# Kernel tuning notes

Hardware: AMD Instinct MI355X
Metric: run time of the kernel (lower is better)

## Reference

```python
import jax, jax.numpy as jnp
import numpy as np

N_HEAD = 16


def setup_inputs() -> dict:
    key = jax.random.key(0)
    ks = jax.random.split(key, 5)
    B, T, C = 4, 4096, 2048
    H = N_HEAD
    x = jax.random.normal(ks[0], (B, T, C), dtype=jnp.float32)
    # torch Linear weights are (out_features, in_features); bias=False
    Wa = jax.random.normal(ks[1], (C, C), dtype=jnp.float32) * 0.02
    Wp = jax.random.normal(ks[2], (C, C), dtype=jnp.float32) * 0.02
    temp = jnp.ones((H, 1), dtype=jnp.float32)
    denom_bias = jnp.zeros((H, T, 1), dtype=jnp.float32)  # block_size == T
    return {"x": x, "Wa": Wa, "Wp": Wp, "temp": temp, "denom_bias": denom_bias}


def reference(x, Wa, Wp, temp, denom_bias):
    B, T, C = x.shape
    H = N_HEAD
    D = C // H
    # c_attn (no bias): y = x @ Wa^T
    w = jnp.einsum('btc,oc->bto', x, Wa)
    w = w.reshape(B, T, H, D).transpose(0, 2, 1, 3)  # (B,H,T,D)
    w_sq = w * w
    # running second-moment denominator along time
    denom = jnp.maximum(jnp.cumsum(w_sq, axis=2), 1e-12)
    w_normed = w_sq / denom + denom_bias[:, :T, :]          # (B,H,T,D)
    tmp = jnp.sum(w_normed, axis=-1) * temp                 # (B,H,T), temp (H,1) broadcasts
    Pi = jax.nn.softmax(tmp, axis=1)                        # softmax over heads
    # token-statistics attention: running Pi-weighted mean of w_sq
    dots = jnp.cumsum(w_sq * Pi[..., None], axis=2) / (jnp.cumsum(Pi, axis=-1) + 1e-8)[..., None]
    attn = 1.0 / (1.0 + dots)                               # (B,H,T,D)
    y = -(w * Pi[..., None]) * attn                         # (B,H,T,D)
    y = y.transpose(0, 2, 1, 3).reshape(B, T, C)
    # c_proj (no bias)
    y = jnp.einsum('btc,oc->bto', y, Wp)
    return y
```

## Files before the change

### kernel.cpp

```cpp
#include <hip/hip_runtime.h>
#include <hip/hip_bf16.h>
#include <stdint.h>

#define BB 4
#define TT 4096
#define CC 2048
#define HH 16
#define DD 128
#define MM (BB*TT)
#define KK CC
#define NNx CC
#define NTP 16

#define NCH 128
#define CHL (TT/NCH)

typedef unsigned short u16;
typedef unsigned int   u32;
typedef __bf16 bf16x8 __attribute__((ext_vector_type(8)));
typedef float  f32x4  __attribute__((ext_vector_type(4)));

__device__ __forceinline__ float bf2f(u32 lo) {
  union { u32 u; float f; } z; z.u = lo << 16; return z.f;
}
__device__ __forceinline__ u16 f2bf(float f) {
  union { float f; u32 u; } z; z.f = f;
  u32 u = z.u;
  return (u16)((u + 0x7FFFu + ((u >> 16) & 1u)) >> 16);
}
__device__ __forceinline__ void unpack8(uint4 v, float* a) {
  a[0]=bf2f(v.x&0xffffu); a[1]=bf2f(v.x>>16);
  a[2]=bf2f(v.y&0xffffu); a[3]=bf2f(v.y>>16);
  a[4]=bf2f(v.z&0xffffu); a[5]=bf2f(v.z>>16);
  a[6]=bf2f(v.w&0xffffu); a[7]=bf2f(v.w>>16);
}

__global__ void cvt_f32_bf16(const float* __restrict__ in, u16* __restrict__ out, long n) {
  long i = ((long)blockIdx.x * blockDim.x + threadIdx.x) * 8;
  if (i >= n) return;
  float4 v0 = *(const float4*)(in + i);
  float4 v1 = *(const float4*)(in + i + 4);
  uint4 o;
  o.x = (u32)f2bf(v0.x) | ((u32)f2bf(v0.y) << 16);
  o.y = (u32)f2bf(v0.z) | ((u32)f2bf(v0.w) << 16);
  o.z = (u32)f2bf(v1.x) | ((u32)f2bf(v1.y) << 16);
  o.w = (u32)f2bf(v1.z) | ((u32)f2bf(v1.w) << 16);
  *(uint4*)(out + i) = o;
}

__device__ __forceinline__ void gload16(const void* g, void* l) {
  __builtin_amdgcn_global_load_lds(
      (__attribute__((address_space(1))) void*)g,
      (__attribute__((address_space(3))) void*)l, 16, 0, 0);
}

template<int OUTF32, int EPI>
__global__ __launch_bounds__(512, 2)
void gemm256(const u16* __restrict__ A, const u16* __restrict__ Bm,
             float* __restrict__ Cf, u16* __restrict__ Cb,
             float* __restrict__ S1)
{
  __shared__ u16 As[4][8192];
  __shared__ u16 Bs[4][8192];
  const int tid  = threadIdx.x;
  const int wid  = tid >> 6;
  const int lane = tid & 63;
  const int wm = wid >> 2, wn = wid & 3;
  const int fr = lane & 15, kg = lane >> 4;
  const int orig = blockIdx.x;
  const int nid  = ((orig & 7) << 6) | (orig >> 3);
  const int m0 = (nid >> 3) * 256;
  const int n0 = (nid & 7) * 256;

  const int srow = tid >> 2;
  const int sc   = (tid & 3) ^ ((srow >> 1) & 3);
  const u16* gA0 = A  + (size_t)(m0 + srow) * KK + sc * 8;
  const u16* gA1 = gA0 + (size_t)128 * KK;
  const u16* gB0 = Bm + (size_t)(n0 + srow) * KK + sc * 8;
  const u16* gB1 = gB0 + (size_t)128 * KK;
  const int ldst0 = wid * 512;
  const int ldst1 = 4096 + wid * 512;

  const int cs    = kg ^ ((fr >> 1) & 3);
  const int abase = (wm * 128 + fr) * 32 + cs * 8;
  const int bbase = (wn * 64  + fr) * 32 + cs * 8;

  f32x4 acc[8][4];
  #pragma unroll
  for (int i = 0; i < 8; ++i)
    #pragma unroll
    for (int j = 0; j < 4; ++j) acc[i][j] = (f32x4){0.f,0.f,0.f,0.f};

  auto stA = [&](int slot, int ko) {
    gload16(gA0 + ko, &As[slot][ldst0]);
    gload16(gA1 + ko, &As[slot][ldst1]);
  };
  auto stB = [&](int slot, int ko) {
    gload16(gB0 + ko, &Bs[slot][ldst0]);
    gload16(gB1 + ko, &Bs[slot][ldst1]);
  };

  stA(0, 0);  stB(0, 0);
  stA(1, 32); stB(1, 32);
  stA(2, 64); stB(2, 64);
  asm volatile("s_waitcnt vmcnt(8)" ::: "memory");
  __builtin_amdgcn_s_barrier();

  bf16x8 av[4], bv[4];

#define PH(CSLOT, MH, LOADB, STMT, DOWAIT) do {                               \
    _Pragma("unroll")                                                         \
    for (int f = 0; f < 4; ++f)                                               \
      av[f] = *(const bf16x8*)&As[CSLOT][abase + ((MH)*64 + f*16)*32];        \
    if (LOADB) {                                                              \
      _Pragma("unroll")                                                       \
      for (int f = 0; f < 4; ++f)                                             \
        bv[f] = *(const bf16x8*)&Bs[CSLOT][bbase + f*16*32];                  \
    }                                                                         \
    STMT;                                                                     \
    if (DOWAIT) asm volatile("s_waitcnt vmcnt(8)" ::: "memory");              \
    __builtin_amdgcn_s_barrier();                                             \
    __builtin_amdgcn_s_setprio(1);                                            \
    _Pragma("unroll")                                                         \
    for (int f = 0; f < 4; ++f)                                               \
      _Pragma("unroll")                                                       \
      for (int n = 0; n < 4; ++n)                                             \
        acc[(MH)*4+f][n] = __builtin_amdgcn_mfma_f32_16x16x32_bf16(          \
            av[f], bv[n], acc[(MH)*4+f][n], 0, 0, 0);                         \
    __builtin_amdgcn_s_setprio(0);                                            \
    __builtin_amdgcn_s_barrier();                                             \
  } while (0)

  for (int it = 0; it < NTP; ++it) {
    const int kb = it * 128;
    const bool nx = (it + 1 < NTP);
    PH(0, 0, 1, stA(3, kb + 96), 0);
    PH(0, 1, 0, stB(3, kb + 96), 1);
    PH(1, 0, 1, if (nx) stA(0, kb + 128), 0);
    PH(1, 1, 0, if (nx) stB(0, kb + 128), 1);
    PH(2, 0, 1, if (nx) stA(1, kb + 160), 0);
    PH(2, 1, 0, if (nx) stB(1, kb + 160), 1);
    PH(3, 0, 1, if (nx) stA(2, kb + 192), 0);
    PH(3, 1, 0, if (nx) stB(2, kb + 192), 1);
  }
#undef PH

  const int row0 = m0 + wm * 128 + kg * 4;
  const int col0 = n0 + wn * 64 + fr;
  if (OUTF32) {
    #pragma unroll
    for (int mf = 0; mf < 8; ++mf)
      #pragma unroll
      for (int nf = 0; nf < 4; ++nf)
        #pragma unroll
        for (int r = 0; r < 4; ++r)
          Cf[(size_t)(row0 + mf*16 + r) * NNx + col0 + nf*16] = acc[mf][nf][r];
  } else {
    float csum[4][4];
    #pragma unroll
    for (int p = 0; p < 4; ++p)
      #pragma unroll
      for (int nf = 0; nf < 4; ++nf) csum[p][nf] = 0.f;
    #pragma unroll
    for (int mf = 0; mf < 8; ++mf)
      #pragma unroll
      for (int nf = 0; nf < 4; ++nf)
        #pragma unroll
        for (int r = 0; r < 4; ++r) {
          u16 hb = f2bf(acc[mf][nf][r]);
          Cb[(size_t)(row0 + mf*16 + r) * NNx + col0 + nf*16] = hb;
          if (EPI) { float av_ = bf2f(hb); csum[mf>>1][nf] += av_ * av_; }
        }
    if (EPI) {
      const int b   = m0 >> 12;
      const int ch0 = ((m0 & (TT-1)) >> 5) + wm * 4;
      #pragma unroll
      for (int p = 0; p < 4; ++p)
        #pragma unroll
        for (int nf = 0; nf < 4; ++nf) {
          float v = csum[p][nf];
          v += __shfl_xor(v, 16, 64);
          v += __shfl_xor(v, 32, 64);
          if (kg == 0)
            S1[(size_t)(ch0 + p) * (BB*CC) + b * CC + col0 + nf*16] = v;
        }
    }
  }
}

__global__ void excl_big(float* __restrict__ p) {
  const int g = blockIdx.x * 256 + threadIdx.x;
  float run = 0.f;
  for (int ch = 0; ch < NCH; ++ch) {
    float v = p[(size_t)ch * (BB*CC) + g];
    p[(size_t)ch * (BB*CC) + g] = run;
    run += v;
  }
}
__global__ void excl_sp(float* __restrict__ p) {
  const int g = threadIdx.x;
  float run = 0.f;
  for (int ch = 0; ch < NCH; ++ch) {
    float v = p[ch * (BB*HH) + g];
    p[ch * (BB*HH) + g] = run;
    run += v;
  }
}

__global__ __launch_bounds__(256)
void pass_c(const u16* __restrict__ w, float* __restrict__ S,
            float* __restrict__ SP, float* __restrict__ Pi,
            const float* __restrict__ temp, const float* __restrict__ dbias)
{
  __shared__ float sm[2][HH];
  const int ch = blockIdx.x, b = blockIdx.y;
  const int tid = threadIdx.x;
  const int h = tid >> 4;
  const int t0 = ch * CHL;
  const u16* wrow = w + ((size_t)b*TT + t0) * CC + tid*8;
  float* Srow = S + (size_t)ch * (BB*CC) + b * CC + tid*8;
  float c0[8], s2[8];
  #pragma unroll
  for (int j = 0; j < 8; ++j) { c0[j] = Srow[j]; s2[j] = 0.f; }
  const float th = temp[h];
  const float* db = dbias + (size_t)h * TT + t0;
  float sp = 0.f;
  uint4 v = *(const uint4*)wrow;
  for (int t = 0; t < CHL; ++t) {
    uint4 vn = v;
    if (t + 1 < CHL) vn = *(const uint4*)(wrow + (size_t)(t+1) * CC);
    float a2[8];
    { float a[8]; unpack8(v, a);
      #pragma unroll
      for (int j = 0; j < 8; ++j) a2[j] = a[j]*a[j]; }
    float val = 0.f;
    #pragma unroll
    for (int j = 0; j < 8; ++j) {
      c0[j] += a2[j];
      val += a2[j] * __builtin_amdgcn_rcpf(fmaxf(c0[j], 1e-12f));
    }
    val += __shfl_xor(val, 1, 64);
    val += __shfl_xor(val, 2, 64);
    val += __shfl_xor(val, 4, 64);
    val += __shfl_xor(val, 8, 64);
    const float tmp = th * (val + (float)DD * db[t]);
    if ((tid & 15) == 0) sm[t & 1][h] = tmp;
    __syncthreads();
    float m = -1e30f;
    #pragma unroll
    for (int hh = 0; hh < HH; ++hh) m = fmaxf(m, sm[t & 1][hh]);
    float ssum = 0.f;
    #pragma unroll
    for (int hh = 0; hh < HH; ++hh) ssum += __expf(sm[t & 1][hh] - m);
    const float pi = __expf(sm[t & 1][h] - m) * __builtin_amdgcn_rcpf(ssum);
    sp += pi;
    #pragma unroll
    for (int j = 0; j < 8; ++j) s2[j] += a2[j] * pi;
    if ((tid & 15) == 0) Pi[((size_t)b*TT + t0 + t) * HH + h] = pi;
    v = vn;
  }
  #pragma unroll
  for (int j = 0; j < 8; ++j) Srow[j] = s2[j];
  if ((tid & 15) == 0) SP[ch * (BB*HH) + b * HH + h] = sp;
}

__global__ __launch_bounds__(256)
void pass_d(const u16* __restrict__ w, const float* __restrict__ S2,
            const float* __restrict__ SP, const float* __restrict__ Pi,
            u16* __restrict__ ymid)
{
  const int ch = blockIdx.x, b = blockIdx.y;
  const int tid = threadIdx.x;
  const int h = tid >> 4;
  const int t0 = ch * CHL;
  const u16* wrow = w + ((size_t)b*TT + t0) * CC + tid*8;
  u16* yrow = ymid + ((size_t)b*TT + t0) * CC + tid*8;
  const float* Srow = S2 + (size_t)ch * (BB*CC) + b * CC + tid*8;
  float c2[8];
  #pragma unroll
  for (int j = 0; j < 8; ++j) c2[j] = Srow[j];
  float cp = SP[ch * (BB*HH) + b * HH + h];
  const float* prow = Pi + ((size_t)b*TT + t0) * HH + h;
  uint4 v = *(const uint4*)wrow;
  for (int t = 0; t < CHL; ++t) {
    uint4 vn = v;
    if (t + 1 < CHL) vn = *(const uint4*)(wrow + (size_t)(t+1) * CC);
    const float pi = prow[(size_t)t * HH];
    cp += pi;
    const float invp = __builtin_amdgcn_rcpf(cp + 1e-8f);
    float a[8]; unpack8(v, a);
    float y[8];
    #pragma unroll
    for (int j = 0; j < 8; ++j) {
      const float a2 = a[j]*a[j];
      c2[j] += a2 * pi;
      const float d = c2[j] * invp;
      y[j] = -(a[j] * pi) * __builtin_amdgcn_rcpf(1.f + d);
    }
    uint4 o;
    o.x = (u32)f2bf(y[0]) | ((u32)f2bf(y[1]) << 16);
    o.y = (u32)f2bf(y[2]) | ((u32)f2bf(y[3]) << 16);
    o.z = (u32)f2bf(y[4]) | ((u32)f2bf(y[5]) << 16);
    o.w = (u32)f2bf(y[6]) | ((u32)f2bf(y[7]) << 16);
    *(uint4*)(yrow + (size_t)t * CC) = o;
    v = vn;
  }
}

extern "C" void kernel_launch(void* const* d_in, const int* in_sizes, int n_in,
                              void* d_out, int out_size, void* d_ws, size_t ws_size,
                              hipStream_t stream) {
  const float* x     = (const float*)d_in[0];
  const float* Wa    = (const float*)d_in[1];
  const float* Wp    = (const float*)d_in[2];
  const float* temp  = (const float*)d_in[3];
  const float* dbias = (const float*)d_in[4];
  float* out = (float*)d_out;

  char* ws = (char*)d_ws;
  u16*  xb   = (u16*)(ws);
  u16*  Wab  = (u16*)(ws + 67108864);
  u16*  Wpb  = (u16*)(ws + 75497472);
  u16*  wbuf = (u16*)(ws + 83886080);
  float* S1  = (float*)(ws + 150994944);
  float* SP  = (float*)(ws + 155189248);
  float* Pi  = (float*)(ws + 67108864);
  u16*  ymid = xb;

  cvt_f32_bf16<<<(MM*(long)KK)/8/256, 256, 0, stream>>>(x,  xb,  (long)MM*KK);
  cvt_f32_bf16<<<((long)CC*CC)/8/256, 256, 0, stream>>>(Wa, Wab, (long)CC*CC);
  cvt_f32_bf16<<<((long)CC*CC)/8/256, 256, 0, stream>>>(Wp, Wpb, (long)CC*CC);

  gemm256<0,1><<<512, 512, 0, stream>>>(xb, Wab, nullptr, wbuf, S1);

  excl_big<<<(BB*CC)/256, 256, 0, stream>>>(S1);

  dim3 gc(NCH, BB);
  pass_c<<<gc, 256, 0, stream>>>(wbuf, S1, SP, Pi, temp, dbias);

  excl_big<<<(BB*CC)/256, 256, 0, stream>>>(S1);
  excl_sp<<<1, 64, 0, stream>>>(SP);

  pass_d<<<gc, 256, 0, stream>>>(wbuf, S1, SP, Pi, ymid);

  gemm256<1,0><<<512, 512, 0, stream>>>(ymid, Wpb, out, nullptr, nullptr);
}
```

Before: 385.7 us.

## Double-buffer LDS fragment registers to overlap ds_reads with MFMA in GEMM loop

Restructures the GEMM main loop to use two sets of A/B register fragments. The next phase's LDS reads are issued before the current phase's MFMA block, so shared-memory latency hides behind matrix math. It also drops one barrier per phase. The cost is extra VGPR pressure from the duplicated fragments, which may reduce occupancy. Barrier placement also changes, and correctness depends on the ordering between slot reuse and the global-to-LDS loads.

```diff
diff --git a/kernel.cpp b/kernel.cpp
--- a/kernel.cpp
+++ b/kernel.cpp
@@ -100,50 +100,82 @@
     gload16(gB1 + ko, &Bs[slot][ldst1]);
   };
 
-  stA(0, 0);  stB(0, 0);
-  stA(1, 32); stB(1, 32);
-  stA(2, 64); stB(2, 64);
-  asm volatile("s_waitcnt vmcnt(8)" ::: "memory");
-  __builtin_amdgcn_s_barrier();
-
-  bf16x8 av[4], bv[4];
-
-#define PH(CSLOT, MH, LOADB, STMT, DOWAIT) do {                               \
+#define LDA4(dst, SLOT, MH)                                                   \
     _Pragma("unroll")                                                         \
     for (int f = 0; f < 4; ++f)                                               \
-      av[f] = *(const bf16x8*)&As[CSLOT][abase + ((MH)*64 + f*16)*32];        \
-    if (LOADB) {                                                              \
-      _Pragma("unroll")                                                       \
-      for (int f = 0; f < 4; ++f)                                             \
-        bv[f] = *(const bf16x8*)&Bs[CSLOT][bbase + f*16*32];                  \
-    }                                                                         \
-    STMT;                                                                     \
-    if (DOWAIT) asm volatile("s_waitcnt vmcnt(8)" ::: "memory");              \
-    __builtin_amdgcn_s_barrier();                                             \
+      dst[f] = *(const bf16x8*)&As[SLOT][abase + ((MH)*64 + f*16)*32];
+#define LDB4(dst, SLOT)                                                       \
+    _Pragma("unroll")                                                         \
+    for (int f = 0; f < 4; ++f)                                               \
+      dst[f] = *(const bf16x8*)&Bs[SLOT][bbase + f*16*32];
+#define MF16(AV, BV, MH)                                                      \
     __builtin_amdgcn_s_setprio(1);                                            \
     _Pragma("unroll")                                                         \
     for (int f = 0; f < 4; ++f)                                               \
       _Pragma("unroll")                                                       \
       for (int n = 0; n < 4; ++n)                                             \
         acc[(MH)*4+f][n] = __builtin_amdgcn_mfma_f32_16x16x32_bf16(          \
-            av[f], bv[n], acc[(MH)*4+f][n], 0, 0, 0);                         \
+            AV[f], BV[n], acc[(MH)*4+f][n], 0, 0, 0);                         \
     __builtin_amdgcn_s_setprio(0);                                            \
-    __builtin_amdgcn_s_barrier();                                             \
-  } while (0)
+    __builtin_amdgcn_s_barrier();
+
+  stA(0, 0);  stB(0, 0);
+  stA(1, 32); stB(1, 32);
+  stA(2, 64); stB(2, 64);
+  asm volatile("s_waitcnt vmcnt(8)" ::: "memory");
+  __builtin_amdgcn_s_barrier();
+
+  bf16x8 a0[4], a1[4], b0[4], b1[4];
+  LDA4(a0, 0, 0)
+  LDB4(b0, 0)
 
   for (int it = 0; it < NTP; ++it) {
     const int kb = it * 128;
     const bool nx = (it + 1 < NTP);
-    PH(0, 0, 1, stA(3, kb + 96), 0);
-    PH(0, 1, 0, stB(3, kb + 96), 1);
-    PH(1, 0, 1, if (nx) stA(0, kb + 128), 0);
-    PH(1, 1, 0, if (nx) stB(0, kb + 128), 1);
-    PH(2, 0, 1, if (nx) stA(1, kb + 160), 0);
-    PH(2, 1, 0, if (nx) stB(1, kb + 160), 1);
-    PH(3, 0, 1, if (nx) stA(2, kb + 192), 0);
-    PH(3, 1, 0, if (nx) stB(2, kb + 192), 1);
-  }
-#undef PH
+    stA(3, kb + 96);
+    __builtin_amdgcn_s_barrier();
+    LDA4(a1, 0, 1)
+    MF16(a0, b0, 0)
+    stB(3, kb + 96);
+    asm volatile("s_waitcnt vmcnt(8)" ::: "memory");
+    __builtin_amdgcn_s_barrier();
+    LDA4(a0, 1, 0)
+    LDB4(b1, 1)
+    MF16(a1, b0, 1)
+    if (nx) stA(0, kb + 128);
+    __builtin_amdgcn_s_barrier();
+    LDA4(a1, 1, 1)
+    MF16(a0, b1, 0)
+    if (nx) stB(0, kb + 128);
+    asm volatile("s_waitcnt vmcnt(8)" ::: "memory");
+    __builtin_amdgcn_s_barrier();
+    LDA4(a0, 2, 0)
+    LDB4(b0, 2)
+    MF16(a1, b1, 1)
+    if (nx) stA(1, kb + 160);
+    __builtin_amdgcn_s_barrier();
+    LDA4(a1, 2, 1)
+    MF16(a0, b0, 0)
+    if (nx) stB(1, kb + 160);
+    asm volatile("s_waitcnt vmcnt(8)" ::: "memory");
+    __builtin_amdgcn_s_barrier();
+    LDA4(a0, 3, 0)
+    LDB4(b1, 3)
+    MF16(a1, b0, 1)
+    if (nx) stA(2, kb + 192);
+    __builtin_amdgcn_s_barrier();
+    LDA4(a1, 3, 1)
+    MF16(a0, b1, 0)
+    if (nx) stB(2, kb + 192);
+    asm volatile("s_waitcnt vmcnt(8)" ::: "memory");
+    __builtin_amdgcn_s_barrier();
+    LDA4(a0, 0, 0)
+    LDB4(b0, 0)
+    MF16(a1, b1, 1)
+  }
+#undef LDA4
+#undef LDB4
+#undef MF16
 
   const int row0 = m0 + wm * 128 + kg * 4;
   const int col0 = n0 + wn * 64 + fr;
```

Result: no change. 392.9 us (+1.9%).

## Restructure GEMM main loop to process two K-slots per phase with fewer barriers

Applied to the files above, without the earlier changes.

Reorganizes the bf16 MFMA GEMM pipeline so each phase loads A/B fragments for two K-slots at once and issues 32 MFMAs between barriers, instead of 16 per phase with eight barrier pairs per iteration. Global-to-LDS prefetches are grouped two slots at a time after an explicit lgkmcnt wait. The goal is to cut barrier and synchronization overhead and give the scheduler longer MFMA runs. In exchange it needs more fragment registers (ak0/ak1/bk0/bk1), which may lower occupancy, and the prefetch distance per slot changes.

```diff
diff --git a/kernel.cpp b/kernel.cpp
--- a/kernel.cpp
+++ b/kernel.cpp
@@ -100,50 +100,74 @@
     gload16(gB1 + ko, &Bs[slot][ldst1]);
   };
 
-  stA(0, 0);  stB(0, 0);
-  stA(1, 32); stB(1, 32);
-  stA(2, 64); stB(2, 64);
-  asm volatile("s_waitcnt vmcnt(8)" ::: "memory");
-  __builtin_amdgcn_s_barrier();
-
-  bf16x8 av[4], bv[4];
-
-#define PH(CSLOT, MH, LOADB, STMT, DOWAIT) do {                               \
+#define LDA4S(dst, SLOT, MH)                                                  \
     _Pragma("unroll")                                                         \
     for (int f = 0; f < 4; ++f)                                               \
-      av[f] = *(const bf16x8*)&As[CSLOT][abase + ((MH)*64 + f*16)*32];        \
-    if (LOADB) {                                                              \
-      _Pragma("unroll")                                                       \
-      for (int f = 0; f < 4; ++f)                                             \
-        bv[f] = *(const bf16x8*)&Bs[CSLOT][bbase + f*16*32];                  \
-    }                                                                         \
-    STMT;                                                                     \
-    if (DOWAIT) asm volatile("s_waitcnt vmcnt(8)" ::: "memory");              \
-    __builtin_amdgcn_s_barrier();                                             \
-    __builtin_amdgcn_s_setprio(1);                                            \
+      dst[f] = *(const bf16x8*)&As[SLOT][abase + ((MH)*64 + f*16)*32];
+#define LDB4S(dst, SLOT)                                                      \
+    _Pragma("unroll")                                                         \
+    for (int f = 0; f < 4; ++f)                                               \
+      dst[f] = *(const bf16x8*)&Bs[SLOT][bbase + f*16*32];
+#define MFHALF(AV, BV, MH)                                                    \
     _Pragma("unroll")                                                         \
     for (int f = 0; f < 4; ++f)                                               \
       _Pragma("unroll")                                                       \
       for (int n = 0; n < 4; ++n)                                             \
         acc[(MH)*4+f][n] = __builtin_amdgcn_mfma_f32_16x16x32_bf16(          \
-            av[f], bv[n], acc[(MH)*4+f][n], 0, 0, 0);                         \
-    __builtin_amdgcn_s_setprio(0);                                            \
-    __builtin_amdgcn_s_barrier();                                             \
-  } while (0)
+            AV[f], BV[n], acc[(MH)*4+f][n], 0, 0, 0);
+
+  stA(0, 0);  stA(1, 32); stB(0, 0);  stB(1, 32);
+  stA(2, 64); stA(3, 96); stB(2, 64); stB(3, 96);
+  asm volatile("s_waitcnt vmcnt(8)" ::: "memory");
+  __builtin_amdgcn_s_barrier();
+
+  bf16x8 ak0[4], ak1[4], bk0[4], bk1[4];
 
   for (int it = 0; it < NTP; ++it) {
     const int kb = it * 128;
     const bool nx = (it + 1 < NTP);
-    PH(0, 0, 1, stA(3, kb + 96), 0);
-    PH(0, 1, 0, stB(3, kb + 96), 1);
-    PH(1, 0, 1, if (nx) stA(0, kb + 128), 0);
-    PH(1, 1, 0, if (nx) stB(0, kb + 128), 1);
-    PH(2, 0, 1, if (nx) stA(1, kb + 160), 0);
-    PH(2, 1, 0, if (nx) stB(1, kb + 160), 1);
-    PH(3, 0, 1, if (nx) stA(2, kb + 192), 0);
-    PH(3, 1, 0, if (nx) stB(2, kb + 192), 1);
-  }
-#undef PH
+    LDA4S(ak0, 0, 0) LDA4S(ak1, 1, 0)
+    LDB4S(bk0, 0)    LDB4S(bk1, 1)
+    __builtin_amdgcn_s_setprio(1);
+    MFHALF(ak0, bk0, 0) MFHALF(ak1, bk1, 0)
+    __builtin_amdgcn_s_setprio(0);
+    LDA4S(ak0, 0, 1) LDA4S(ak1, 1, 1)
+    asm volatile("s_waitcnt lgkmcnt(0)" ::: "memory");
+    __builtin_amdgcn_s_barrier();
+    if (nx) {
+      stA(0, kb + 128); stA(1, kb + 160);
+      stB(0, kb + 128); stB(1, kb + 160);
+      asm volatile("s_waitcnt vmcnt(8)" ::: "memory");
+    } else {
+      asm volatile("s_waitcnt vmcnt(0)" ::: "memory");
+    }
+    __builtin_amdgcn_s_barrier();
+    __builtin_amdgcn_s_setprio(1);
+    MFHALF(ak0, bk0, 1) MFHALF(ak1, bk1, 1)
+    __builtin_amdgcn_s_setprio(0);
+    LDA4S(ak0, 2, 0) LDA4S(ak1, 3, 0)
+    LDB4S(bk0, 2)    LDB4S(bk1, 3)
+    __builtin_amdgcn_s_setprio(1);
+    MFHALF(ak0, bk0, 0) MFHALF(ak1, bk1, 0)
+    __builtin_amdgcn_s_setprio(0);
+    LDA4S(ak0, 2, 1) LDA4S(ak1, 3, 1)
+    asm volatile("s_waitcnt lgkmcnt(0)" ::: "memory");
+    __builtin_amdgcn_s_barrier();
+    if (nx) {
+      stA(2, kb + 192); stA(3, kb + 224);
+      stB(2, kb + 192); stB(3, kb + 224);
+      asm volatile("s_waitcnt vmcnt(8)" ::: "memory");
+    } else {
+      asm volatile("s_waitcnt vmcnt(0)" ::: "memory");
+    }
+    __builtin_amdgcn_s_barrier();
+    __builtin_amdgcn_s_setprio(1);
+    MFHALF(ak0, bk0, 1) MFHALF(ak1, bk1, 1)
+    __builtin_amdgcn_s_setprio(0);
+  }
+#undef LDA4S
+#undef LDB4S
+#undef MFHALF
 
   const int row0 = m0 + wm * 128 + kg * 4;
   const int col0 = n0 + wn * 64 + fr;
```

Result: no change. 383.1 us (-0.7%).

## Fuse fp32-to-bf16 conversion of x into first GEMM's A-tile loading

Applied to the files above, without the earlier changes.

The first GEMM now reads fp32 x directly through registers, converts it to bf16 in-kernel and writes it to LDS, with register double-buffering (U/V) prefetched two stages ahead. This removes the standalone conversion pass over the 128 MB activation tensor, along with its write and re-read of the bf16 copy. The two weight conversions are merged into a single launch. The cost is double the global read bytes for A inside the GEMM, VGPR pressure from the staging registers, and ALU work spent on conversion in the MFMA loop.

```diff
diff --git a/kernel.cpp b/kernel.cpp
--- a/kernel.cpp
+++ b/kernel.cpp
@@ -28,6 +28,11 @@
   u32 u = z.u;
   return (u16)((u + 0x7FFFu + ((u >> 16) & 1u)) >> 16);
 }
+__device__ __forceinline__ u32 pk2(u32 a, u32 b) {
+  u32 ra = (a + 0x7FFFu + ((a >> 16) & 1u)) >> 16;
+  u32 rb = (b + 0x7FFFu + ((b >> 16) & 1u)) >> 16;
+  return ra | (rb << 16);
+}
 __device__ __forceinline__ void unpack8(uint4 v, float* a) {
   a[0]=bf2f(v.x&0xffffu); a[1]=bf2f(v.x>>16);
   a[2]=bf2f(v.y&0xffffu); a[3]=bf2f(v.y>>16);
@@ -35,17 +40,21 @@
   a[6]=bf2f(v.w&0xffffu); a[7]=bf2f(v.w>>16);
 }
 
-__global__ void cvt_f32_bf16(const float* __restrict__ in, u16* __restrict__ out, long n) {
+__global__ void cvt_w2(const float* __restrict__ wa, const float* __restrict__ wp,
+                       u16* __restrict__ oa, u16* __restrict__ op) {
+  const long n = (long)CC * CC;
   long i = ((long)blockIdx.x * blockDim.x + threadIdx.x) * 8;
-  if (i >= n) return;
-  float4 v0 = *(const float4*)(in + i);
-  float4 v1 = *(const float4*)(in + i + 4);
+  const float* in = (i < n) ? wa : wp;
+  u16* out = (i < n) ? oa : op;
+  long j = (i < n) ? i : i - n;
+  float4 v0 = *(const float4*)(in + j);
+  float4 v1 = *(const float4*)(in + j + 4);
   uint4 o;
   o.x = (u32)f2bf(v0.x) | ((u32)f2bf(v0.y) << 16);
   o.y = (u32)f2bf(v0.z) | ((u32)f2bf(v0.w) << 16);
   o.z = (u32)f2bf(v1.x) | ((u32)f2bf(v1.y) << 16);
   o.w = (u32)f2bf(v1.z) | ((u32)f2bf(v1.w) << 16);
-  *(uint4*)(out + i) = o;
+  *(uint4*)(out + j) = o;
 }
 
 __device__ __forceinline__ void gload16(const void* g, void* l) {
@@ -54,9 +63,10 @@
       (__attribute__((address_space(3))) void*)l, 16, 0, 0);
 }
 
-template<int OUTF32, int EPI>
+template<int OUTF32, int EPI, int AF32>
 __global__ __launch_bounds__(512, 2)
-void gemm256(const u16* __restrict__ A, const u16* __restrict__ Bm,
+void gemm256(const float* __restrict__ Af, const u16* __restrict__ Ab,
+             const u16* __restrict__ Bm,
              float* __restrict__ Cf, u16* __restrict__ Cb,
              float* __restrict__ S1)
 {
@@ -74,8 +84,10 @@
 
   const int srow = tid >> 2;
   const int sc   = (tid & 3) ^ ((srow >> 1) & 3);
-  const u16* gA0 = A  + (size_t)(m0 + srow) * KK + sc * 8;
-  const u16* gA1 = gA0 + (size_t)128 * KK;
+  const u16*  gA0 = Ab + (size_t)(m0 + srow) * KK + sc * 8;
+  const u16*  gA1 = gA0 + (size_t)128 * KK;
+  const float* fA0 = Af + (size_t)(m0 + srow) * KK + sc * 8;
+  const float* fA1 = fA0 + (size_t)128 * KK;
   const u16* gB0 = Bm + (size_t)(n0 + srow) * KK + sc * 8;
   const u16* gB1 = gB0 + (size_t)128 * KK;
   const int ldst0 = wid * 512;
@@ -92,33 +104,41 @@
     for (int j = 0; j < 4; ++j) acc[i][j] = (f32x4){0.f,0.f,0.f,0.f};
 
   auto stA = [&](int slot, int ko) {
+    ko = (ko < KK) ? ko : 0;
     gload16(gA0 + ko, &As[slot][ldst0]);
     gload16(gA1 + ko, &As[slot][ldst1]);
   };
   auto stB = [&](int slot, int ko) {
+    ko = (ko < KK) ? ko : 0;
     gload16(gB0 + ko, &Bs[slot][ldst0]);
     gload16(gB1 + ko, &Bs[slot][ldst1]);
   };
-
-  stA(0, 0);  stB(0, 0);
-  stA(1, 32); stB(1, 32);
-  stA(2, 64); stB(2, 64);
-  asm volatile("s_waitcnt vmcnt(8)" ::: "memory");
-  __builtin_amdgcn_s_barrier();
-
-  bf16x8 av[4], bv[4];
-
-#define PH(CSLOT, MH, LOADB, STMT, DOWAIT) do {                               \
+  uint4 U[4], V[4];
+  auto aload = [&](uint4* g, int ko) {
+    int kc = (ko < KK) ? ko : 0;
+    g[0] = *(const uint4*)(fA0 + kc); g[1] = *(const uint4*)(fA0 + kc + 4);
+    g[2] = *(const uint4*)(fA1 + kc); g[3] = *(const uint4*)(fA1 + kc + 4);
+  };
+  auto awrite = [&](int slot, uint4* g) {
+    uint4 o0, o1;
+    o0.x = pk2(g[0].x, g[0].y); o0.y = pk2(g[0].z, g[0].w);
+    o0.z = pk2(g[1].x, g[1].y); o0.w = pk2(g[1].z, g[1].w);
+    o1.x = pk2(g[2].x, g[2].y); o1.y = pk2(g[2].z, g[2].w);
+    o1.z = pk2(g[3].x, g[3].y); o1.w = pk2(g[3].z, g[3].w);
+    *(uint4*)&As[slot][ldst0 + lane * 8] = o0;
+    *(uint4*)&As[slot][ldst1 + lane * 8] = o1;
+  };
+
+#define LDA4S(SLOT, MH)                                                       \
     _Pragma("unroll")                                                         \
     for (int f = 0; f < 4; ++f)                                               \
-      av[f] = *(const bf16x8*)&As[CSLOT][abase + ((MH)*64 + f*16)*32];        \
-    if (LOADB) {                                                              \
-      _Pragma("unroll")                                                       \
-      for (int f = 0; f < 4; ++f)                                             \
-        bv[f] = *(const bf16x8*)&Bs[CSLOT][bbase + f*16*32];                  \
-    }                                                                         \
-    STMT;                                                                     \
-    if (DOWAIT) asm volatile("s_waitcnt vmcnt(8)" ::: "memory");              \
+      av[f] = *(const bf16x8*)&As[SLOT][abase + ((MH)*64 + f*16)*32];
+#define LDB4S(SLOT)                                                           \
+    _Pragma("unroll")                                                         \
+    for (int f = 0; f < 4; ++f)                                               \
+      bv[f] = *(const bf16x8*)&Bs[SLOT][bbase + f*16*32];
+#define WAIT8 asm volatile("s_waitcnt vmcnt(8)" ::: "memory");
+#define BARMF(MH)                                                             \
     __builtin_amdgcn_s_barrier();                                             \
     __builtin_amdgcn_s_setprio(1);                                            \
     _Pragma("unroll")                                                         \
@@ -128,22 +148,66 @@
         acc[(MH)*4+f][n] = __builtin_amdgcn_mfma_f32_16x16x32_bf16(          \
             av[f], bv[n], acc[(MH)*4+f][n], 0, 0, 0);                         \
     __builtin_amdgcn_s_setprio(0);                                            \
-    __builtin_amdgcn_s_barrier();                                             \
-  } while (0)
+    __builtin_amdgcn_s_barrier();
+
+  if constexpr (AF32) {
+    aload(U, 0);  asm volatile("s_waitcnt vmcnt(0)" ::: "memory"); awrite(0, U);
+    aload(U, 32); asm volatile("s_waitcnt vmcnt(0)" ::: "memory"); awrite(1, U);
+    aload(U, 64); asm volatile("s_waitcnt vmcnt(0)" ::: "memory"); awrite(2, U);
+    aload(U, 96);
+    aload(V, 128);
+    stB(0, 0); stB(1, 32); stB(2, 64);
+    asm volatile("s_waitcnt vmcnt(4)" ::: "memory");
+    asm volatile("s_waitcnt lgkmcnt(0)" ::: "memory");
+  } else {
+    stA(0, 0);  stB(0, 0);
+    stA(1, 32); stB(1, 32);
+    stA(2, 64); stB(2, 64);
+    asm volatile("s_waitcnt vmcnt(8)" ::: "memory");
+  }
+  __builtin_amdgcn_s_barrier();
+
+  bf16x8 av[4], bv[4];
 
   for (int it = 0; it < NTP; ++it) {
     const int kb = it * 128;
-    const bool nx = (it + 1 < NTP);
-    PH(0, 0, 1, stA(3, kb + 96), 0);
-    PH(0, 1, 0, stB(3, kb + 96), 1);
-    PH(1, 0, 1, if (nx) stA(0, kb + 128), 0);
-    PH(1, 1, 0, if (nx) stB(0, kb + 128), 1);
-    PH(2, 0, 1, if (nx) stA(1, kb + 160), 0);
-    PH(2, 1, 0, if (nx) stB(1, kb + 160), 1);
-    PH(3, 0, 1, if (nx) stA(2, kb + 192), 0);
-    PH(3, 1, 0, if (nx) stB(2, kb + 192), 1);
-  }
-#undef PH
+    if constexpr (AF32) { awrite(3, U); aload(U, kb + 160); }
+    else                { stA(3, kb + 96); }
+    LDA4S(0, 0) LDB4S(0)
+    BARMF(0)
+    LDA4S(0, 1)
+    stB(3, kb + 96);
+    WAIT8
+    BARMF(1)
+    if constexpr (AF32) { awrite(0, V); aload(V, kb + 192); }
+    else                { stA(0, kb + 128); }
+    LDA4S(1, 0) LDB4S(1)
+    BARMF(0)
+    LDA4S(1, 1)
+    stB(0, kb + 128);
+    WAIT8
+    BARMF(1)
+    if constexpr (AF32) { awrite(1, U); aload(U, kb + 224); }
+    else                { stA(1, kb + 160); }
+    LDA4S(2, 0) LDB4S(2)
+    BARMF(0)
+    LDA4S(2, 1)
+    stB(1, kb + 160);
+    WAIT8
+    BARMF(1)
+    if constexpr (AF32) { awrite(2, V); aload(V, kb + 256); }
+    else                { stA(2, kb + 192); }
+    LDA4S(3, 0) LDB4S(3)
+    BARMF(0)
+    LDA4S(3, 1)
+    stB(2, kb + 192);
+    WAIT8
+    BARMF(1)
+  }
+#undef LDA4S
+#undef LDB4S
+#undef WAIT8
+#undef BARMF
 
   const int row0 = m0 + wm * 128 + kg * 4;
   const int col0 = n0 + wn * 64 + fr;
@@ -318,20 +382,17 @@
   float* out = (float*)d_out;
 
   char* ws = (char*)d_ws;
-  u16*  xb   = (u16*)(ws);
+  u16*  ymid = (u16*)(ws);
   u16*  Wab  = (u16*)(ws + 67108864);
   u16*  Wpb  = (u16*)(ws + 75497472);
   u16*  wbuf = (u16*)(ws + 83886080);
   float* S1  = (float*)(ws + 150994944);
   float* SP  = (float*)(ws + 155189248);
   float* Pi  = (float*)(ws + 67108864);
-  u16*  ymid = xb;
-
-  cvt_f32_bf16<<<(MM*(long)KK)/8/256, 256, 0, stream>>>(x,  xb,  (long)MM*KK);
-  cvt_f32_bf16<<<((long)CC*CC)/8/256, 256, 0, stream>>>(Wa, Wab, (long)CC*CC);
-  cvt_f32_bf16<<<((long)CC*CC)/8/256, 256, 0, stream>>>(Wp, Wpb, (long)CC*CC);
-
-  gemm256<0,1><<<512, 512, 0, stream>>>(xb, Wab, nullptr, wbuf, S1);
+
+  cvt_w2<<<(2L*CC*CC)/8/256, 256, 0, stream>>>(Wa, Wp, Wab, Wpb);
+
+  gemm256<0,1,1><<<512, 512, 0, stream>>>(x, nullptr, Wab, nullptr, wbuf, S1);
 
   excl_big<<<(BB*CC)/256, 256, 0, stream>>>(S1);
 
@@ -343,5 +404,5 @@
 
   pass_d<<<gc, 256, 0, stream>>>(wbuf, S1, SP, Pi, ymid);
 
-  gemm256<1,0><<<512, 512, 0, stream>>>(ymid, Wpb, out, nullptr, nullptr);
-}
+  gemm256<1,0,0><<<512, 512, 0, stream>>>(nullptr, ymid, Wpb, out, nullptr, nullptr);
+}
```

New measurement: 420.7 us. +9.1%, slower.
